# Performance work log

Measured on AMD Instinct MI355X. Metric: run time of the kernel, lower is better.

The kernel has to match this reference:

```python
import jax, jax.numpy as jnp
import numpy as np

N_HEADS = 8

def setup_inputs() -> dict:
    key = jax.random.key(0)
    ks = jax.random.split(key, 12)
    B, S2, C, H, W = 2, 2048, 1280, 256, 256
    s = 0.02  # weight init scale
    return {
        'hidden_states': jax.random.normal(ks[0], (B, S2, C), dtype=jnp.float32),
        'src_mask': (jax.random.uniform(ks[1], (B, 1, H, W)) > 0.5).astype(jnp.float32),
        'attn_wq': jax.random.normal(ks[2], (C, C), dtype=jnp.float32) * s,
        'attn_wk': jax.random.normal(ks[3], (C, C), dtype=jnp.float32) * s,
        'attn_wv': jax.random.normal(ks[4], (C, C), dtype=jnp.float32) * s,
        'out_w': jax.random.normal(ks[5], (C, C), dtype=jnp.float32) * s,
        'out_b': jnp.zeros((C,), dtype=jnp.float32),
        'proc_wq': jax.random.normal(ks[6], (C, C), dtype=jnp.float32) * s,
        'proc_wk': jax.random.normal(ks[7], (C, C), dtype=jnp.float32) * s,
        'proc_wv': jax.random.normal(ks[8], (C, C), dtype=jnp.float32) * s,
        'ww': jax.random.normal(ks[9], (C + 1, 1), dtype=jnp.float32) * s,
        'wb': jnp.zeros((1,), dtype=jnp.float32),
    }


def reference(hidden_states, src_mask, attn_wq, attn_wk, attn_wv, out_w, out_b,
              proc_wq, proc_wk, proc_wv, ww, wb):
    B, S2, C = hidden_states.shape
    S = S2 // 2  # condition_flag=False: sequence is two images concatenated
    _, _, H, W = src_mask.shape
    r = int(np.sqrt((H * W) / S))  # nearest-neighbor downsample ratio
    # F.interpolate(mode='nearest') with exact integer ratio == strided slice
    m = src_mask[:, 0, ::r, ::r].reshape(B, S, 1)          # [B, S, 1]
    mask = jnp.concatenate([m, m], axis=1)                 # [B, 2S, 1]
    # sigmoid gate blending the two query projections
    gate_in = jnp.concatenate([hidden_states, mask], axis=-1)  # [B, 2S, C+1]
    w = jax.nn.sigmoid(gate_in @ ww + wb)                  # [B, 2S, 1]
    query = (hidden_states @ attn_wq) * w + (hidden_states @ proc_wq) * (1.0 - w)
    # keys/values: first half through attn's projections, second half through processor's
    e1, e2 = hidden_states[:, :S], hidden_states[:, S:]
    key = jnp.concatenate([e1 @ attn_wk, e2 @ proc_wk], axis=1)
    value = jnp.concatenate([e1 @ attn_wv, e2 @ proc_wv], axis=1)
    d = C // N_HEADS
    def split_heads(x):
        return x.reshape(B, S2, N_HEADS, d).transpose(0, 2, 1, 3)  # [B, H, S2, d]
    qh, kh, vh = split_heads(query), split_heads(key), split_heads(value)
    scale = float(1.0 / np.sqrt(d))
    scores = jnp.einsum('bhqd,bhkd->bhqk', qh, kh) * scale
    probs = jax.nn.softmax(scores, axis=-1)
    out = jnp.einsum('bhqk,bhkd->bhqd', probs, vh)
    out = out.transpose(0, 2, 1, 3).reshape(B, S2, C)
    out = out @ out_w + out_b
    # residual connection, rescale_output_factor == 1
    return out + hidden_states
```

## Files before the change

kernel.cpp:

```cpp
#include <hip/hip_runtime.h>

typedef unsigned short u16;
typedef u16 u16x4 __attribute__((ext_vector_type(4)));
typedef u16 u16x8 __attribute__((ext_vector_type(8)));
typedef __bf16 bf16x8 __attribute__((ext_vector_type(8)));
typedef float f32x4 __attribute__((ext_vector_type(4)));

#define DEVI __device__ __forceinline__

#if __has_builtin(__builtin_amdgcn_exp2f)
#define EXP2F __builtin_amdgcn_exp2f
#else
#define EXP2F exp2f
#endif

DEVI u16 f2b(float f) {
  unsigned u = __builtin_bit_cast(unsigned, f);
  u += 0x7fffu + ((u >> 16) & 1u);
  return (u16)(u >> 16);
}

DEVI float b2f(u16 v) { return __builtin_bit_cast(float, (unsigned)v << 16); }

DEVI f32x4 mfma16(u16x8 a, u16x8 b, f32x4 c) {
  return __builtin_amdgcn_mfma_f32_16x16x32_bf16(
      __builtin_bit_cast(bf16x8, a), __builtin_bit_cast(bf16x8, b), c, 0, 0, 0);
}

DEVI void async_copy16(const u16* g, u16* l) {
  __builtin_amdgcn_global_load_lds(
      (__attribute__((address_space(1))) unsigned int*)(g),
      (__attribute__((address_space(3))) unsigned int*)(l), 16, 0, 0);
}

DEVI void fence_barrier() {
  asm volatile("" ::: "memory");
  __builtin_amdgcn_s_barrier();
  asm volatile("" ::: "memory");
}

__global__ void prep_kernel(const float* __restrict__ hs, const float* __restrict__ mask,
                            const float* __restrict__ ww, const float* __restrict__ wb,
                            u16* __restrict__ hsb, float* __restrict__ wgate) {
  int token = blockIdx.x;
  int tid = threadIdx.x;
  const float* row = hs + (size_t)token * 1280;
  u16* orow = hsb + (size_t)token * 1280;
  float acc = 0.f;
#pragma unroll
  for (int i = 0; i < 5; i++) {
    int c = i * 256 + tid;
    float v = row[c];
    orow[c] = f2b(v);
    acc += v * ww[c];
  }
#pragma unroll
  for (int off = 1; off < 64; off <<= 1) acc += __shfl_xor(acc, off);
  __shared__ float partial[4];
  int wid = tid >> 6;
  if ((tid & 63) == 0) partial[wid] = acc;
  __syncthreads();
  if (tid == 0) {
    float tot = partial[0] + partial[1] + partial[2] + partial[3];
    int b = token >> 11, t = token & 2047;
    int s = t & 1023;
    float mv = mask[b * 65536 + ((s >> 5) * 8) * 256 + (s & 31) * 8];
    float z = tot + mv * ww[1280] + wb[0];
    wgate[token] = 1.f / (1.f + __expf(-z));
  }
}

__global__ void wtrans_kernel(const float* w0, const float* w1, const float* w2,
                              const float* w3, const float* w4, const float* w5,
                              const float* w6, u16* __restrict__ out) {
  const float* src;
  switch (blockIdx.z) {
    case 0: src = w0; break; case 1: src = w1; break; case 2: src = w2; break;
    case 3: src = w3; break; case 4: src = w4; break; case 5: src = w5; break;
    default: src = w6; break;
  }
  u16* dst = out + (size_t)blockIdx.z * 1280 * 1280;
  __shared__ float tile[32][33];
  int tx = threadIdx.x & 31, ty = threadIdx.x >> 5;
  int k0 = blockIdx.x * 32, n0 = blockIdx.y * 32;
#pragma unroll
  for (int r = 0; r < 4; r++)
    tile[ty + r * 8][tx] = src[(size_t)(k0 + ty + r * 8) * 1280 + n0 + tx];
  __syncthreads();
#pragma unroll
  for (int r = 0; r < 4; r++)
    dst[(size_t)(n0 + ty + r * 8) * 1280 + k0 + tx] = f2b(tile[tx][ty + r * 8]);
}

__launch_bounds__(256)
__global__ void gemm_qkv_kernel(const u16* __restrict__ A, const u16* __restrict__ Wt,
                                u16* __restrict__ Qa, u16* __restrict__ Qp,
                                u16* __restrict__ Kout, u16* __restrict__ VTout) {
  const int K = 1280, N = 1280;
  const size_t WSZ = (size_t)1280 * 1280;
  __shared__ u16 As[128 * 32];
  __shared__ u16 Bs[128 * 32];

  int tid = threadIdx.x;
  int wid = tid >> 6, lane = tid & 63;
  int nb = blockIdx.x, mb = blockIdx.y, z = blockIdx.z;
  int m0 = mb * 128, n0 = nb * 128;
  bool first = ((m0 & 2047) < 1024);

  const u16* B;
  switch (z) {
    case 0:  B = Wt + 0 * WSZ; break;
    case 1:  B = Wt + 4 * WSZ; break;
    case 2:  B = first ? Wt + 1 * WSZ : Wt + 5 * WSZ; break;
    default: B = first ? Wt + 2 * WSZ : Wt + 6 * WSZ; break;
  }

  f32x4 zero = {0.f, 0.f, 0.f, 0.f};
  f32x4 acc[4][4];
#pragma unroll
  for (int i = 0; i < 4; i++)
#pragma unroll
    for (int j = 0; j < 4; j++) acc[i][j] = zero;

  int wr = wid >> 1, wc = wid & 1;

  for (int kk = 0; kk < 40; kk++) {
    int k0 = kk * 32;
#pragma unroll
    for (int i = 0; i < 2; i++) {
      int slot = i * 256 + tid;
      int row = slot >> 2, seg = slot & 3;
      async_copy16(A + (size_t)(m0 + row) * K + k0 + seg * 8, As + (size_t)(i * 256 + wid * 64) * 8);
      async_copy16(B + (size_t)(n0 + row) * K + k0 + seg * 8, Bs + (size_t)(i * 256 + wid * 64) * 8);
    }
    asm volatile("s_waitcnt vmcnt(0)" ::: "memory");
    __syncthreads();

    u16x8 af[4], bfr[4];
#pragma unroll
    for (int mi = 0; mi < 4; mi++)
      af[mi] = *(const u16x8*)(As + (wr * 64 + mi * 16 + (lane & 15)) * 32 + (lane >> 4) * 8);
#pragma unroll
    for (int ni = 0; ni < 4; ni++)
      bfr[ni] = *(const u16x8*)(Bs + (wc * 64 + ni * 16 + (lane & 15)) * 32 + (lane >> 4) * 8);
#pragma unroll
    for (int mi = 0; mi < 4; mi++)
#pragma unroll
      for (int ni = 0; ni < 4; ni++)
        acc[mi][ni] = mfma16(af[mi], bfr[ni], acc[mi][ni]);
    __syncthreads();
  }

  if (z == 3) {
#pragma unroll
    for (int mi = 0; mi < 4; mi++)
#pragma unroll
      for (int ni = 0; ni < 4; ni++) {
        int row0 = m0 + wr * 64 + mi * 16 + ((lane >> 4) << 2);
        int col = n0 + wc * 64 + ni * 16 + (lane & 15);
        int b = row0 >> 11, s = row0 & 2047;
        int h = col / 160, c_in = col - h * 160;
        u16x4 v = {f2b(acc[mi][ni][0]), f2b(acc[mi][ni][1]),
                   f2b(acc[mi][ni][2]), f2b(acc[mi][ni][3])};
        *(u16x4*)(VTout + ((size_t)(b * 8 + h) * 160 + c_in) * 2048 + s) = v;
      }
  } else {
    u16* Cb = (z == 0) ? Qa : (z == 1) ? Qp : Kout;
#pragma unroll
    for (int mi = 0; mi < 4; mi++)
#pragma unroll
      for (int ni = 0; ni < 4; ni++)
#pragma unroll
        for (int r = 0; r < 4; r++) {
          int row = m0 + wr * 64 + mi * 16 + ((lane >> 4) << 2) + r;
          int col = n0 + wc * 64 + ni * 16 + (lane & 15);
          Cb[(size_t)row * N + col] = f2b(acc[mi][ni][r]);
        }
  }
}

__global__ void qblend_kernel(u16* __restrict__ Qa, const u16* __restrict__ Qp,
                              const float* __restrict__ wgate, float qscale) {
  int idx = blockIdx.x * 256 + threadIdx.x;
  int token = idx / 160;
  float w = wgate[token];
  u16x8 qa = *(const u16x8*)(Qa + (size_t)idx * 8);
  u16x8 qp = *(const u16x8*)(Qp + (size_t)idx * 8);
  u16x8 o;
#pragma unroll
  for (int j = 0; j < 8; j++)
    o[j] = f2b((w * b2f(qa[j]) + (1.f - w) * b2f(qp[j])) * qscale);
  *(u16x8*)(Qa + (size_t)idx * 8) = o;
}

template <int SPLIT>
__launch_bounds__(256)
__global__ void flash_kernel(const u16* __restrict__ Q, const u16* __restrict__ Kg,
                             const u16* __restrict__ VTg, u16* __restrict__ O,
                             u16* __restrict__ Opart, float* __restrict__ MLbuf) {
  const int C = 1280;
  int bid = blockIdx.x;
  int qb = bid & 31, h = (bid >> 5) & 7, b = bid >> 8;
  int sp = (SPLIT > 1) ? (int)blockIdx.y : 0;
  int tid = threadIdx.x, wid = tid >> 6, lane = tid & 63;

  int t0, NT;
  if (SPLIT == 3) { t0 = sp * 11; NT = (sp < 2) ? 11 : 10; }
  else if (SPLIT == 1) { t0 = 0; NT = 32; }
  else { t0 = sp * (32 / SPLIT); NT = 32 / SPLIT; }

  const size_t baseQ = ((size_t)(b * 2048 + qb * 64)) * C + h * 160;
  const size_t baseK = ((size_t)(b * 2048)) * C + h * 160;
  const size_t baseVT = (size_t)(b * 8 + h) * 160 * 2048;

  __shared__ u16 Ks[64 * 168];
  __shared__ u16 Vts[160 * 64];
  __shared__ u16 Psh[4 * 16 * 40];

  const u16* kbase = Kg + baseK + (size_t)(t0 * 64) * C;
  const u16* vbase = VTg + baseVT + t0 * 64;
  unsigned koff[6], kld[6];
#pragma unroll
  for (int j = 0; j < 6; j++) {
    int i = wid + 4 * j;
    if (i > 20) i = wid + 16;
    int gc = i * 64 + lane;
    int r = gc / 21, ch = gc - r * 21;
    int chs = ch < 20 ? ch : 19;
    koff[j] = (unsigned)(r * C + chs * 8);
    kld[j] = (unsigned)(i * 512);
  }
  unsigned voff[5], vld[5];
#pragma unroll
  for (int j = 0; j < 5; j++) {
    int i = wid + 4 * j;
    int gc = i * 64 + lane;
    int c = gc >> 3, jj = gc & 7;
    voff[j] = (unsigned)(c * 2048 + ((jj ^ (c & 7)) << 3));
    vld[j] = (unsigned)(i * 512);
  }

#define STAGE_K()                                   \
  do {                                              \
    _Pragma("unroll") for (int j = 0; j < 6; j++)   \
        async_copy16(kbase + koff[j], Ks + kld[j]); \
  } while (0)
#define STAGE_V()                                    \
  do {                                               \
    _Pragma("unroll") for (int j = 0; j < 5; j++)    \
        async_copy16(vbase + voff[j], Vts + vld[j]); \
  } while (0)

  u16x8 qf[5];
  {
    int row = wid * 16 + (lane & 15);
    const u16* qrow = Q + baseQ + (size_t)row * C;
#pragma unroll
    for (int ks = 0; ks < 5; ks++)
      qf[ks] = *(const u16x8*)(qrow + ks * 32 + (lane >> 4) * 8);
  }

  f32x4 zero = {0.f, 0.f, 0.f, 0.f};
  f32x4 oacc[10];
#pragma unroll
  for (int i = 0; i < 10; i++) oacc[i] = zero;
  float mrow[4], lrow[4];
#pragma unroll
  for (int r = 0; r < 4; r++) { mrow[r] = -1e30f; lrow[r] = 0.f; }

  STAGE_K();
  STAGE_V();

  for (int kti = 0; kti < NT; kti++) {
    bool last = (kti == NT - 1);
    asm volatile("s_waitcnt vmcnt(5)" ::: "memory");
    fence_barrier();

    f32x4 sc[4];
#pragma unroll
    for (int ct = 0; ct < 4; ct++) {
      f32x4 a = zero;
#pragma unroll
      for (int ks = 0; ks < 5; ks++) {
        u16x8 kf = *(const u16x8*)(&Ks[(ct * 16 + (lane & 15)) * 168 + ks * 32 + (lane >> 4) * 8]);
        a = mfma16(qf[ks], kf, a);
      }
      sc[ct] = a;
    }

    fence_barrier();
    if (!last) { kbase += 64 * C; STAGE_K(); }

    float mx[4];
#pragma unroll
    for (int r = 0; r < 4; r++) {
      float m = fmaxf(fmaxf(sc[0][r], sc[1][r]), fmaxf(sc[2][r], sc[3][r]));
#pragma unroll
      for (int off = 1; off < 16; off <<= 1) m = fmaxf(m, __shfl_xor(m, off));
      mx[r] = m;
    }
    bool need = (mx[0] > mrow[0] + 8.f) || (mx[1] > mrow[1] + 8.f) ||
                (mx[2] > mrow[2] + 8.f) || (mx[3] > mrow[3] + 8.f);
    if (__any(need)) {
#pragma unroll
      for (int r = 0; r < 4; r++) {
        float mnew = fmaxf(mrow[r], mx[r]);
        float alpha = EXP2F(mrow[r] - mnew);
        mrow[r] = mnew;
        float rs = 0.f;
#pragma unroll
        for (int ct = 0; ct < 4; ct++) {
          float p = EXP2F(sc[ct][r] - mnew);
          sc[ct][r] = p;
          rs += p;
        }
        lrow[r] = lrow[r] * alpha + rs;
#pragma unroll
        for (int ci = 0; ci < 10; ci++) oacc[ci][r] *= alpha;
      }
    } else {
#pragma unroll
      for (int r = 0; r < 4; r++) {
        float rs = 0.f;
#pragma unroll
        for (int ct = 0; ct < 4; ct++) {
          float p = EXP2F(sc[ct][r] - mrow[r]);
          sc[ct][r] = p;
          rs += p;
        }
        lrow[r] += rs;
      }
    }

    if (!last) { asm volatile("s_waitcnt vmcnt(6)" ::: "memory"); }
    else       { asm volatile("s_waitcnt vmcnt(0)" ::: "memory"); }
    fence_barrier();

#pragma unroll
    for (int kt2 = 0; kt2 < 2; kt2++) {
#pragma unroll
      for (int c2 = 0; c2 < 2; c2++) {
        int ct = kt2 * 2 + c2;
#pragma unroll
        for (int r = 0; r < 4; r++)
          Psh[wid * 640 + ((((lane >> 4) << 2) + r) * 40) + c2 * 16 + (lane & 15)] =
              f2b(sc[ct][r]);
      }
      u16x8 pf = *(const u16x8*)(&Psh[wid * 640 + (lane & 15) * 40 + (lane >> 4) * 8]);
#pragma unroll
      for (int ci = 0; ci < 10; ci++) {
        int c = ci * 16 + (lane & 15);
        int jl = kt2 * 4 + (lane >> 4);
        u16x8 vf = *(const u16x8*)(&Vts[c * 64 + ((jl ^ (c & 7)) << 3)]);
        oacc[ci] = mfma16(pf, vf, oacc[ci]);
      }
    }

    fence_barrier();
    if (!last) { vbase += 64; STAGE_V(); }
  }
#undef STAGE_K
#undef STAGE_V

#pragma unroll
  for (int r = 0; r < 4; r++)
#pragma unroll
    for (int off = 1; off < 16; off <<= 1) lrow[r] += __shfl_xor(lrow[r], off);

  int row0 = qb * 64 + wid * 16 + ((lane >> 4) << 2);
  if constexpr (SPLIT > 1) {
    float linv[4];
#pragma unroll
    for (int r = 0; r < 4; r++) linv[r] = 1.f / lrow[r];
    size_t g0 = (size_t)sp * 4096 + (size_t)b * 2048 + row0;
#pragma unroll
    for (int ci = 0; ci < 10; ci++) {
      int col = h * 160 + ci * 16 + (lane & 15);
#pragma unroll
      for (int r = 0; r < 4; r++)
        Opart[(g0 + r) * 1280 + col] = f2b(oacc[ci][r] * linv[r]);
    }
    if ((lane & 15) == 0) {
#pragma unroll
      for (int r = 0; r < 4; r++) {
        size_t mi = ((g0 + r) * 8 + h) * 2;
        MLbuf[mi] = mrow[r];
        MLbuf[mi + 1] = lrow[r];
      }
    }
  } else {
#pragma unroll
    for (int ci = 0; ci < 10; ci++) {
      int col = h * 160 + ci * 16 + (lane & 15);
#pragma unroll
      for (int r = 0; r < 4; r++) {
        float v = oacc[ci][r] / lrow[r];
        O[((size_t)(b * 2048) + row0 + r) * C + col] = f2b(v);
      }
    }
  }
}

__global__ void combine_kernel(const u16* __restrict__ Opart, const float* __restrict__ MLbuf,
                               u16* __restrict__ O) {
  int idx = blockIdx.x * 256 + threadIdx.x;
  int token = idx / 160;
  int h = (idx - token * 160) / 20;
  size_t i0 = ((size_t)token * 8 + h) * 2;
  const size_t MLP = (size_t)4096 * 16;
  float m0 = MLbuf[i0], l0 = MLbuf[i0 + 1];
  float m1 = MLbuf[i0 + MLP], l1 = MLbuf[i0 + MLP + 1];
  float m2 = MLbuf[i0 + 2 * MLP], l2 = MLbuf[i0 + 2 * MLP + 1];
  float m = fmaxf(fmaxf(m0, m1), m2);
  float w0 = EXP2F(m0 - m) * l0, w1 = EXP2F(m1 - m) * l1, w2 = EXP2F(m2 - m) * l2;
  float inv = 1.f / (w0 + w1 + w2);
  w0 *= inv; w1 *= inv; w2 *= inv;
  const size_t OPP = (size_t)655360;
  u16x8 a = *(const u16x8*)(Opart + (size_t)idx * 8);
  u16x8 c = *(const u16x8*)(Opart + (OPP + idx) * 8);
  u16x8 d = *(const u16x8*)(Opart + (2 * OPP + idx) * 8);
  u16x8 o;
#pragma unroll
  for (int j = 0; j < 8; j++)
    o[j] = f2b(b2f(a[j]) * w0 + b2f(c[j]) * w1 + b2f(d[j]) * w2);
  *(u16x8*)(O + (size_t)idx * 8) = o;
}

__launch_bounds__(256)
__global__ void gemm_out_kernel(const u16* __restrict__ A, const u16* __restrict__ Bt,
                                float* __restrict__ Cf, const float* __restrict__ bias,
                                const float* __restrict__ resid) {
  const int K = 1280, N = 1280;
  __shared__ u16 As[128 * 32];
  __shared__ u16 Bs[128 * 32];

  int tid = threadIdx.x;
  int wid = tid >> 6, lane = tid & 63;
  int nb = blockIdx.x, mb = blockIdx.y;
  int m0 = mb * 128, n0 = nb * 128;

  f32x4 zero = {0.f, 0.f, 0.f, 0.f};
  f32x4 acc[4][4];
#pragma unroll
  for (int i = 0; i < 4; i++)
#pragma unroll
    for (int j = 0; j < 4; j++) acc[i][j] = zero;

  int wr = wid >> 1, wc = wid & 1;

  for (int kk = 0; kk < 40; kk++) {
    int k0 = kk * 32;
#pragma unroll
    for (int i = 0; i < 2; i++) {
      int slot = i * 256 + tid;
      int row = slot >> 2, seg = slot & 3;
      async_copy16(A + (size_t)(m0 + row) * K + k0 + seg * 8, As + (size_t)(i * 256 + wid * 64) * 8);
      async_copy16(Bt + (size_t)(n0 + row) * K + k0 + seg * 8, Bs + (size_t)(i * 256 + wid * 64) * 8);
    }
    asm volatile("s_waitcnt vmcnt(0)" ::: "memory");
    __syncthreads();

    u16x8 af[4], bfr[4];
#pragma unroll
    for (int mi = 0; mi < 4; mi++)
      af[mi] = *(const u16x8*)(As + (wr * 64 + mi * 16 + (lane & 15)) * 32 + (lane >> 4) * 8);
#pragma unroll
    for (int ni = 0; ni < 4; ni++)
      bfr[ni] = *(const u16x8*)(Bs + (wc * 64 + ni * 16 + (lane & 15)) * 32 + (lane >> 4) * 8);
#pragma unroll
    for (int mi = 0; mi < 4; mi++)
#pragma unroll
      for (int ni = 0; ni < 4; ni++)
        acc[mi][ni] = mfma16(af[mi], bfr[ni], acc[mi][ni]);
    __syncthreads();
  }

#pragma unroll
  for (int mi = 0; mi < 4; mi++)
#pragma unroll
    for (int ni = 0; ni < 4; ni++)
#pragma unroll
      for (int r = 0; r < 4; r++) {
        int row = m0 + wr * 64 + mi * 16 + ((lane >> 4) << 2) + r;
        int col = n0 + wc * 64 + ni * 16 + (lane & 15);
        Cf[(size_t)row * N + col] = acc[mi][ni][r] + bias[col] + resid[(size_t)row * N + col];
      }
}

extern "C" void kernel_launch(void* const* d_in, const int* in_sizes, int n_in,
                              void* d_out, int out_size, void* d_ws, size_t ws_size,
                              hipStream_t stream) {
  const float* hs      = (const float*)d_in[0];
  const float* mask    = (const float*)d_in[1];
  const float* attn_wq = (const float*)d_in[2];
  const float* attn_wk = (const float*)d_in[3];
  const float* attn_wv = (const float*)d_in[4];
  const float* out_w   = (const float*)d_in[5];
  const float* out_b   = (const float*)d_in[6];
  const float* proc_wq = (const float*)d_in[7];
  const float* proc_wk = (const float*)d_in[8];
  const float* proc_wv = (const float*)d_in[9];
  const float* ww      = (const float*)d_in[10];
  const float* wb      = (const float*)d_in[11];
  float* out = (float*)d_out;

  char* ws = (char*)d_ws;
  const size_t TOK = (size_t)4096 * 1280;
  u16* hsb = (u16*)(ws);
  u16* Qb  = (u16*)(ws + 2 * TOK);
  u16* Kb  = (u16*)(ws + 4 * TOK);
  u16* VTb = (u16*)(ws + 6 * TOK);
  u16* AOb = (u16*)(ws + 8 * TOK);
  u16* Wt  = (u16*)(ws + 10 * TOK);
  float* wgate = (float*)(ws + 10 * TOK + (size_t)7 * 1280 * 1280 * 2);
  char* extra = ws + 10 * TOK + (size_t)7 * 1280 * 1280 * 2 + 16384;
  u16* Opart = (u16*)extra;
  float* MLbuf = (float*)(extra + (size_t)3 * 4096 * 1280 * 2);
  size_t need = (size_t)(extra - ws) + (size_t)3 * 4096 * 1280 * 2 + (size_t)3 * 4096 * 8 * 8;

  prep_kernel<<<4096, 256, 0, stream>>>(hs, mask, ww, wb, hsb, wgate);
  wtrans_kernel<<<dim3(40, 40, 7), 256, 0, stream>>>(attn_wq, attn_wk, attn_wv, out_w,
                                                     proc_wq, proc_wk, proc_wv, Wt);
  const size_t WSZ = (size_t)1280 * 1280;
  gemm_qkv_kernel<<<dim3(10, 32, 4), 256, 0, stream>>>(hsb, Wt, Qb, AOb, Kb, VTb);
  const float qscale = 0.11405505533858971f;
  qblend_kernel<<<2560, 256, 0, stream>>>(Qb, AOb, wgate, qscale);

  if (ws_size >= need) {
    flash_kernel<3><<<dim3(512, 3), 256, 0, stream>>>(Qb, Kb, VTb, nullptr, Opart, MLbuf);
    combine_kernel<<<2560, 256, 0, stream>>>(Opart, MLbuf, AOb);
  } else {
    flash_kernel<1><<<dim3(512, 1), 256, 0, stream>>>(Qb, Kb, VTb, AOb, nullptr, nullptr);
  }
  gemm_out_kernel<<<dim3(10, 32), 256, 0, stream>>>(AOb, Wt + 3 * WSZ, out, out_b, hs);
}
```

Measured before the change: 250.9 us.

## Transpose attention MFMA layout so softmax stats stay per-lane and P moves via bpermute

Swaps the MFMA operand order so each lane holds one query row's scores across four keys. Row max and sum then need only two cross-lane shuffles instead of four per row, and the m/l state shrinks to one scalar per lane. The P tile reaches the PV MFMA through packed bf16 conversion and ds_bpermute instead of an LDS store, read and barrier-free round trip. Output stores become 4-wide vector writes. The cost is more bpermute traffic and a lane-permutation mapping that must exactly match the MFMA operand layout.

```diff
diff --git a/kernel.cpp b/kernel.cpp
--- a/kernel.cpp
+++ b/kernel.cpp
@@ -5,6 +5,7 @@
 typedef u16 u16x8 __attribute__((ext_vector_type(8)));
 typedef __bf16 bf16x8 __attribute__((ext_vector_type(8)));
 typedef float f32x4 __attribute__((ext_vector_type(4)));
+typedef unsigned u32x4 __attribute__((ext_vector_type(4)));
 
 #define DEVI __device__ __forceinline__
 
@@ -21,6 +22,12 @@
 }
 
 DEVI float b2f(u16 v) { return __builtin_bit_cast(float, (unsigned)v << 16); }
+
+DEVI unsigned cvtpk_bf16(float lo, float hi) {
+  unsigned r;
+  asm("v_cvt_pk_bf16_f32 %0, %1, %2" : "=v"(r) : "v"(lo), "v"(hi));
+  return r;
+}
 
 DEVI f32x4 mfma16(u16x8 a, u16x8 b, f32x4 c) {
   return __builtin_amdgcn_mfma_f32_16x16x32_bf16(
@@ -215,11 +222,10 @@
 
   __shared__ u16 Ks[64 * 168];
   __shared__ u16 Vts[160 * 64];
-  __shared__ u16 Psh[4 * 16 * 40];
 
   const u16* kbase = Kg + baseK + (size_t)(t0 * 64) * C;
   const u16* vbase = VTg + baseVT + t0 * 64;
-  unsigned koff[6], kld[6];
+  unsigned koff[6];
 #pragma unroll
   for (int j = 0; j < 6; j++) {
     int i = wid + 4 * j;
@@ -228,28 +234,33 @@
     int r = gc / 21, ch = gc - r * 21;
     int chs = ch < 20 ? ch : 19;
     koff[j] = (unsigned)(r * C + chs * 8);
-    kld[j] = (unsigned)(i * 512);
-  }
-  unsigned voff[5], vld[5];
+  }
+  unsigned voff[5];
 #pragma unroll
   for (int j = 0; j < 5; j++) {
     int i = wid + 4 * j;
     int gc = i * 64 + lane;
     int c = gc >> 3, jj = gc & 7;
     voff[j] = (unsigned)(c * 2048 + ((jj ^ (c & 7)) << 3));
-    vld[j] = (unsigned)(i * 512);
-  }
-
-#define STAGE_K()                                   \
-  do {                                              \
-    _Pragma("unroll") for (int j = 0; j < 6; j++)   \
-        async_copy16(kbase + koff[j], Ks + kld[j]); \
+  }
+
+#define STAGE_K()                                       \
+  do {                                                  \
+    _Pragma("unroll") for (int j = 0; j < 6; j++) {     \
+      int i = wid + 4 * j;                              \
+      if (i > 20) i = wid + 16;                         \
+      async_copy16(kbase + koff[j], Ks + i * 512);      \
+    }                                                   \
   } while (0)
-#define STAGE_V()                                    \
-  do {                                               \
-    _Pragma("unroll") for (int j = 0; j < 5; j++)    \
-        async_copy16(vbase + voff[j], Vts + vld[j]); \
+#define STAGE_V()                                               \
+  do {                                                          \
+    _Pragma("unroll") for (int j = 0; j < 5; j++)               \
+        async_copy16(vbase + voff[j], Vts + (wid + 4 * j) * 512); \
   } while (0)
+
+  const int addr0 = ((lane & 15) + 16 * (((lane >> 4) * 2 + 0) & 3)) << 2;
+  const int addr1 = ((lane & 15) + 16 * (((lane >> 4) * 2 + 1) & 3)) << 2;
+  const bool hihalf = (lane >= 32);
 
   u16x8 qf[5];
   {
@@ -264,9 +275,7 @@
   f32x4 oacc[10];
 #pragma unroll
   for (int i = 0; i < 10; i++) oacc[i] = zero;
-  float mrow[4], lrow[4];
-#pragma unroll
-  for (int r = 0; r < 4; r++) { mrow[r] = -1e30f; lrow[r] = 0.f; }
+  float mrow = -1e30f, lrow = 0.f;
 
   STAGE_K();
   STAGE_V();
@@ -283,7 +292,7 @@
 #pragma unroll
       for (int ks = 0; ks < 5; ks++) {
         u16x8 kf = *(const u16x8*)(&Ks[(ct * 16 + (lane & 15)) * 168 + ks * 32 + (lane >> 4) * 8]);
-        a = mfma16(qf[ks], kf, a);
+        a = mfma16(kf, qf[ks], a);
       }
       sc[ct] = a;
     }
@@ -291,45 +300,48 @@
     fence_barrier();
     if (!last) { kbase += 64 * C; STAGE_K(); }
 
-    float mx[4];
-#pragma unroll
-    for (int r = 0; r < 4; r++) {
-      float m = fmaxf(fmaxf(sc[0][r], sc[1][r]), fmaxf(sc[2][r], sc[3][r]));
-#pragma unroll
-      for (int off = 1; off < 16; off <<= 1) m = fmaxf(m, __shfl_xor(m, off));
-      mx[r] = m;
-    }
-    bool need = (mx[0] > mrow[0] + 8.f) || (mx[1] > mrow[1] + 8.f) ||
-                (mx[2] > mrow[2] + 8.f) || (mx[3] > mrow[3] + 8.f);
-    if (__any(need)) {
-#pragma unroll
-      for (int r = 0; r < 4; r++) {
-        float mnew = fmaxf(mrow[r], mx[r]);
-        float alpha = EXP2F(mrow[r] - mnew);
-        mrow[r] = mnew;
-        float rs = 0.f;
-#pragma unroll
-        for (int ct = 0; ct < 4; ct++) {
+    float m = sc[0][0];
+#pragma unroll
+    for (int ct = 0; ct < 4; ct++)
+#pragma unroll
+      for (int r = 0; r < 4; r++) m = fmaxf(m, sc[ct][r]);
+    m = fmaxf(m, __shfl_xor(m, 16));
+    m = fmaxf(m, __shfl_xor(m, 32));
+
+    if (__any(m > mrow + 8.f)) {
+      float mnew = fmaxf(mrow, m);
+      float alpha = EXP2F(mrow - mnew);
+      mrow = mnew;
+      float rs = 0.f;
+#pragma unroll
+      for (int ct = 0; ct < 4; ct++)
+#pragma unroll
+        for (int r = 0; r < 4; r++) {
           float p = EXP2F(sc[ct][r] - mnew);
           sc[ct][r] = p;
           rs += p;
         }
-        lrow[r] = lrow[r] * alpha + rs;
-#pragma unroll
-        for (int ci = 0; ci < 10; ci++) oacc[ci][r] *= alpha;
-      }
+      lrow = lrow * alpha + rs;
+#pragma unroll
+      for (int ci = 0; ci < 10; ci++) oacc[ci] *= alpha;
     } else {
-#pragma unroll
-      for (int r = 0; r < 4; r++) {
-        float rs = 0.f;
-#pragma unroll
-        for (int ct = 0; ct < 4; ct++) {
-          float p = EXP2F(sc[ct][r] - mrow[r]);
+      float rs = 0.f;
+#pragma unroll
+      for (int ct = 0; ct < 4; ct++)
+#pragma unroll
+        for (int r = 0; r < 4; r++) {
+          float p = EXP2F(sc[ct][r] - mrow);
           sc[ct][r] = p;
           rs += p;
         }
-        lrow[r] += rs;
-      }
+      lrow += rs;
+    }
+
+    unsigned pk0[4], pk1[4];
+#pragma unroll
+    for (int ct = 0; ct < 4; ct++) {
+      pk0[ct] = cvtpk_bf16(sc[ct][0], sc[ct][1]);
+      pk1[ct] = cvtpk_bf16(sc[ct][2], sc[ct][3]);
     }
 
     if (!last) { asm volatile("s_waitcnt vmcnt(6)" ::: "memory"); }
@@ -338,21 +350,27 @@
 
 #pragma unroll
     for (int kt2 = 0; kt2 < 2; kt2++) {
-#pragma unroll
-      for (int c2 = 0; c2 < 2; c2++) {
-        int ct = kt2 * 2 + c2;
-#pragma unroll
-        for (int r = 0; r < 4; r++)
-          Psh[wid * 640 + ((((lane >> 4) << 2) + r) * 40) + c2 * 16 + (lane & 15)] =
-              f2b(sc[ct][r]);
-      }
-      u16x8 pf = *(const u16x8*)(&Psh[wid * 640 + (lane & 15) * 40 + (lane >> 4) * 8]);
+      const int cA = kt2 * 2, cB = kt2 * 2 + 1;
+      int a0 = __builtin_amdgcn_ds_bpermute(addr0, (int)pk0[cA]);
+      int a1 = __builtin_amdgcn_ds_bpermute(addr0, (int)pk1[cA]);
+      int a2 = __builtin_amdgcn_ds_bpermute(addr1, (int)pk0[cA]);
+      int a3 = __builtin_amdgcn_ds_bpermute(addr1, (int)pk1[cA]);
+      int b0 = __builtin_amdgcn_ds_bpermute(addr0, (int)pk0[cB]);
+      int b1 = __builtin_amdgcn_ds_bpermute(addr0, (int)pk1[cB]);
+      int b2 = __builtin_amdgcn_ds_bpermute(addr1, (int)pk0[cB]);
+      int b3 = __builtin_amdgcn_ds_bpermute(addr1, (int)pk1[cB]);
+      u32x4 d;
+      d[0] = (unsigned)(hihalf ? b0 : a0);
+      d[1] = (unsigned)(hihalf ? b1 : a1);
+      d[2] = (unsigned)(hihalf ? b2 : a2);
+      d[3] = (unsigned)(hihalf ? b3 : a3);
+      u16x8 pf = __builtin_bit_cast(u16x8, d);
 #pragma unroll
       for (int ci = 0; ci < 10; ci++) {
         int c = ci * 16 + (lane & 15);
         int jl = kt2 * 4 + (lane >> 4);
         u16x8 vf = *(const u16x8*)(&Vts[c * 64 + ((jl ^ (c & 7)) << 3)]);
-        oacc[ci] = mfma16(pf, vf, oacc[ci]);
+        oacc[ci] = mfma16(vf, pf, oacc[ci]);
       }
     }
 
@@ -362,41 +380,32 @@
 #undef STAGE_K
 #undef STAGE_V
 
-#pragma unroll
-  for (int r = 0; r < 4; r++)
-#pragma unroll
-    for (int off = 1; off < 16; off <<= 1) lrow[r] += __shfl_xor(lrow[r], off);
-
-  int row0 = qb * 64 + wid * 16 + ((lane >> 4) << 2);
+  lrow += __shfl_xor(lrow, 16);
+  lrow += __shfl_xor(lrow, 32);
+  float linv = 1.f / lrow;
+
+  int qrow = qb * 64 + wid * 16 + (lane & 15);
   if constexpr (SPLIT > 1) {
-    float linv[4];
-#pragma unroll
-    for (int r = 0; r < 4; r++) linv[r] = 1.f / lrow[r];
-    size_t g0 = (size_t)sp * 4096 + (size_t)b * 2048 + row0;
+    size_t g0 = (size_t)sp * 4096 + (size_t)b * 2048 + qrow;
 #pragma unroll
     for (int ci = 0; ci < 10; ci++) {
-      int col = h * 160 + ci * 16 + (lane & 15);
-#pragma unroll
-      for (int r = 0; r < 4; r++)
-        Opart[(g0 + r) * 1280 + col] = f2b(oacc[ci][r] * linv[r]);
-    }
-    if ((lane & 15) == 0) {
-#pragma unroll
-      for (int r = 0; r < 4; r++) {
-        size_t mi = ((g0 + r) * 8 + h) * 2;
-        MLbuf[mi] = mrow[r];
-        MLbuf[mi + 1] = lrow[r];
-      }
+      int col = h * 160 + ci * 16 + ((lane >> 4) << 2);
+      u16x4 v = {f2b(oacc[ci][0] * linv), f2b(oacc[ci][1] * linv),
+                 f2b(oacc[ci][2] * linv), f2b(oacc[ci][3] * linv)};
+      *(u16x4*)(Opart + g0 * 1280 + col) = v;
+    }
+    if (lane < 16) {
+      size_t mi = (g0 * 8 + h) * 2;
+      MLbuf[mi] = mrow;
+      MLbuf[mi + 1] = lrow;
     }
   } else {
 #pragma unroll
     for (int ci = 0; ci < 10; ci++) {
-      int col = h * 160 + ci * 16 + (lane & 15);
-#pragma unroll
-      for (int r = 0; r < 4; r++) {
-        float v = oacc[ci][r] / lrow[r];
-        O[((size_t)(b * 2048) + row0 + r) * C + col] = f2b(v);
-      }
+      int col = h * 160 + ci * 16 + ((lane >> 4) << 2);
+      u16x4 v = {f2b(oacc[ci][0] * linv), f2b(oacc[ci][1] * linv),
+                 f2b(oacc[ci][2] * linv), f2b(oacc[ci][3] * linv)};
+      *(u16x4*)(O + ((size_t)(b * 2048) + qrow) * C + col) = v;
     }
   }
 }
```

New measurement: 240.4 us. -4.2%, faster.
